# Performance work log

Hardware: AMD Instinct MI355X
Metric: run time of the kernel (lower is better)

Reference implementation:

```python
import jax, jax.numpy as jnp
import numpy as np

N_HEADS = 16
N_KV_HEADS = 4
WINDOW = 128
THETA = 10000.0


def _rope_cos_sin(T, half):
    inv = 1.0 / (THETA ** (jnp.arange(half, dtype=jnp.float32) / half))
    f = jnp.arange(T, dtype=jnp.float32)[:, None] * inv[None, :]  # (T, half)
    return jnp.cos(f), jnp.sin(f)


def _apply_rope(x, cos, sin):
    # x: (B, H, T, hd); interleaved (real, imag) pairs like torch view_as_complex
    xr, xi = x[..., 0::2], x[..., 1::2]
    out_r = xr * cos - xi * sin
    out_i = xr * sin + xi * cos
    return jnp.stack([out_r, out_i], axis=-1).reshape(x.shape)


def setup_inputs() -> dict:
    key = jax.random.key(0)
    ks = jax.random.split(key, 6)
    B, T, C = 1, 4096, 2048
    kvC = (C // N_HEADS) * N_KV_HEADS
    return {
        "x": jax.random.normal(ks[0], (B, T, C), dtype=jnp.float32),
        "wq": jax.random.normal(ks[1], (C, C), dtype=jnp.float32) * 0.02,
        "wk": jax.random.normal(ks[2], (C, kvC), dtype=jnp.float32) * 0.02,
        "wv": jax.random.normal(ks[3], (C, kvC), dtype=jnp.float32) * 0.02,
        "wo": jax.random.normal(ks[4], (C, C), dtype=jnp.float32) * 0.02,
        "sink": jnp.zeros((1, N_HEADS, 1, 1), dtype=jnp.float32),
    }


def reference(x, wq, wk, wv, wo, sink):
    B, T, C = x.shape
    hd = C // N_HEADS
    n_rep = N_HEADS // N_KV_HEADS

    q = (x @ wq).reshape(B, T, N_HEADS, hd).transpose(0, 2, 1, 3)    # (B,H,T,hd)
    k = (x @ wk).reshape(B, T, N_KV_HEADS, hd).transpose(0, 2, 1, 3)  # (B,Hkv,T,hd)
    v = (x @ wv).reshape(B, T, N_KV_HEADS, hd).transpose(0, 2, 1, 3)

    cos, sin = _rope_cos_sin(T, hd // 2)  # (T, hd/2), broadcasts over (B,H,T,hd/2)
    q = _apply_rope(q, cos, sin)
    k = _apply_rope(k, cos, sin)

    # GQA head expansion (repeat_interleave over head dim)
    k = jnp.repeat(k, n_rep, axis=1)
    v = jnp.repeat(v, n_rep, axis=1)

    att = jnp.einsum("bhqd,bhkd->bhqk", q, k) * (hd ** -0.5) + sink

    # symmetric sliding-window band: |i - j| <= window//2
    idx = jnp.arange(T)
    band = jnp.abs(idx[:, None] - idx[None, :]) <= (WINDOW // 2)
    att = jnp.where(band[None, None, :, :], att, -jnp.inf)

    att = jax.nn.softmax(att, axis=-1)
    # torch code replaces NaN rows (fully-masked) with uniform; band always has diag so no-op
    att = jnp.where(jnp.isnan(att), 1.0 / T, att)

    out = jnp.einsum("bhqk,bhkd->bqhd", att, v).reshape(B, T, C)
    return out @ wo
```

## Files before the change

### kernel.cpp

```cpp
#include <hip/hip_runtime.h>
#include <stdint.h>

#define T_SEQ 4096
#define C_DIM 2048
#define HD 128

typedef unsigned short ushort_t;
typedef __attribute__((ext_vector_type(8))) short shortx8;
typedef __attribute__((ext_vector_type(4))) float floatx4;
typedef __attribute__((ext_vector_type(8))) unsigned short u16x8;
typedef __attribute__((ext_vector_type(4))) unsigned short u16x4;

__device__ __forceinline__ ushort_t f2bf(float f) {
  union { float f; uint32_t u; } v; v.f = f;
  v.u += 0x7fffu + ((v.u >> 16) & 1u);
  return (ushort_t)(v.u >> 16);
}
__device__ __forceinline__ void load_lds16(const ushort_t* g, ushort_t* l) {
  __builtin_amdgcn_global_load_lds(
      (const __attribute__((address_space(1))) unsigned int*)g,
      (__attribute__((address_space(3))) unsigned int*)l, 16, 0, 0);
}

__global__ __launch_bounds__(256) void transpose_cvt(
    const float* __restrict__ src, ushort_t* __restrict__ dst, int R, int C) {
  __shared__ float tile[64][65];
  const int c0 = blockIdx.x * 64, r0 = blockIdx.y * 64;
  const int tid = threadIdx.x;
  for (int i = tid; i < 1024; i += 256) {
    int r = i >> 4, cc = (i & 15) * 4;
    float4 v = *(const float4*)&src[(size_t)(r0 + r) * C + c0 + cc];
    tile[r][cc] = v.x; tile[r][cc + 1] = v.y; tile[r][cc + 2] = v.z; tile[r][cc + 3] = v.w;
  }
  __syncthreads();
  for (int i = tid; i < 512; i += 256) {
    int oc = i >> 3;
    int g = (i & 7) * 8;
    u16x8 o;
    for (int j = 0; j < 8; ++j) o[j] = f2bf(tile[g + j][oc]);
    *(u16x8*)&dst[(size_t)(c0 + oc) * R + r0 + g] = o;
  }
}

__global__ __launch_bounds__(256) void cvt_bf16(
    const float* __restrict__ src, ushort_t* __restrict__ dst, int n4) {
  int i = blockIdx.x * 256 + threadIdx.x;
  if (i >= n4) return;
  float4 v = ((const float4*)src)[i];
  u16x4 o; o[0] = f2bf(v.x); o[1] = f2bf(v.y); o[2] = f2bf(v.z); o[3] = f2bf(v.w);
  ((u16x4*)dst)[i] = o;
}

__global__ __launch_bounds__(256, 3) void gemm_qkv(
    const ushort_t* __restrict__ A, const ushort_t* __restrict__ Bt,
    ushort_t* __restrict__ qbb, ushort_t* __restrict__ kbb,
    ushort_t* __restrict__ vtb) {
  __shared__ __align__(16) ushort_t As[128 * 32];
  __shared__ __align__(16) ushort_t Bs[128 * 32];
  const int tid = threadIdx.x;
  const int lane = tid & 63;
  const int wave = tid >> 6;
  const int quad = lane >> 4;
  const int l16 = lane & 15;
  const int m0 = blockIdx.y * 128;
  const int n0 = blockIdx.x * 128;
  const int wm = (wave & 1) * 64;
  const int wn = (wave >> 1) * 64;
  const int K = 2048;

  floatx4 acc[4][4] = {};

  int a_off[4], b_off[4];
  const int sfrag = (quad + ((l16 >> 1) & 3)) & 3;
  for (int i = 0; i < 4; ++i) {
    a_off[i] = (wm + i * 16 + l16) * 32 + sfrag * 8;
    b_off[i] = (wn + i * 16 + l16) * 32 + sfrag * 8;
  }

  for (int kk = 0; kk < 64; ++kk) {
    const int k0 = kk << 5;
    for (int r = 0; r < 2; ++r) {
      int c = r * 256 + tid;
      int row = c >> 2;
      int s = c & 3;
      int g = (s - (row >> 1)) & 3;
      const ushort_t* ga = A + (size_t)(m0 + row) * K + k0 + g * 8;
      const ushort_t* gb = Bt + (size_t)(n0 + row) * K + k0 + g * 8;
      ushort_t* la = As + (size_t)(r * 256 + (tid & 192)) * 8;
      ushort_t* lb = Bs + (size_t)(r * 256 + (tid & 192)) * 8;
      load_lds16(ga, la);
      load_lds16(gb, lb);
    }
    __syncthreads();
    shortx8 af[4], bfr[4];
    for (int i = 0; i < 4; ++i) {
      af[i] = *(const shortx8*)(As + a_off[i]);
      bfr[i] = *(const shortx8*)(Bs + b_off[i]);
    }
    for (int i = 0; i < 4; ++i)
      for (int j = 0; j < 4; ++j)
        acc[i][j] = __builtin_amdgcn_mfma_f32_16x16x32_bf16(af[i], bfr[j], acc[i][j], 0, 0, 0);
    __syncthreads();
  }

  if (blockIdx.x < 20) {
    const bool isq = (blockIdx.x < 16);
    const int par = l16 & 1;
    for (int j = 0; j < 4; ++j) {
      int col = n0 + wn + j * 16 + l16;
      int irot = (col & 127) >> 1;
      float inv = __expf(-0.14391157f * (float)irot);
      for (int i = 0; i < 4; ++i) {
        int t0r = m0 + wm + i * 16 + quad * 4;
        for (int r = 0; r < 4; ++r) {
          float val = acc[i][j][r];
          float other = __shfl_xor(val, 1, 64);
          float sn, cs;
          __sincosf((float)(t0r + r) * inv, &sn, &cs);
          float outv = par ? (other * sn + val * cs) : (val * cs - other * sn);
          if (isq) qbb[(size_t)(t0r + r) * 2048 + col] = f2bf(outv);
          else     kbb[(size_t)(t0r + r) * 512 + (col - 2048)] = f2bf(outv);
        }
      }
    }
  } else {
    for (int j = 0; j < 4; ++j) {
      int dim = n0 + wn + j * 16 + l16 - 2560;
      for (int i = 0; i < 4; ++i) {
        int t0r = m0 + wm + i * 16 + quad * 4;
        u16x4 o;
        for (int r = 0; r < 4; ++r) o[r] = f2bf(acc[i][j][r]);
        *(u16x4*)&vtb[(size_t)dim * T_SEQ + t0r] = o;
      }
    }
  }
}

__global__ __launch_bounds__(256, 3) void gemm_bf16(
    const ushort_t* __restrict__ A, const ushort_t* __restrict__ Bt,
    float* __restrict__ C, int M, int N, int K) {
  __shared__ __align__(16) ushort_t As[128 * 32];
  __shared__ __align__(16) ushort_t Bs[128 * 32];
  const int tid = threadIdx.x;
  const int lane = tid & 63;
  const int wave = tid >> 6;
  const int quad = lane >> 4;
  const int l16 = lane & 15;
  const int m0 = blockIdx.y * 128;
  const int n0 = blockIdx.x * 128;
  const int wm = (wave & 1) * 64;
  const int wn = (wave >> 1) * 64;

  floatx4 acc[4][4] = {};

  int a_off[4], b_off[4];
  const int sfrag = (quad + ((l16 >> 1) & 3)) & 3;
  for (int i = 0; i < 4; ++i) {
    a_off[i] = (wm + i * 16 + l16) * 32 + sfrag * 8;
    b_off[i] = (wn + i * 16 + l16) * 32 + sfrag * 8;
  }

  const int nk = K >> 5;
  for (int kk = 0; kk < nk; ++kk) {
    const int k0 = kk << 5;
    for (int r = 0; r < 2; ++r) {
      int c = r * 256 + tid;
      int row = c >> 2;
      int s = c & 3;
      int g = (s - (row >> 1)) & 3;
      const ushort_t* ga = A + (size_t)(m0 + row) * K + k0 + g * 8;
      const ushort_t* gb = Bt + (size_t)(n0 + row) * K + k0 + g * 8;
      ushort_t* la = As + (size_t)(r * 256 + (tid & 192)) * 8;
      ushort_t* lb = Bs + (size_t)(r * 256 + (tid & 192)) * 8;
      load_lds16(ga, la);
      load_lds16(gb, lb);
    }
    __syncthreads();
    shortx8 af[4], bfr[4];
    for (int i = 0; i < 4; ++i) {
      af[i] = *(const shortx8*)(As + a_off[i]);
      bfr[i] = *(const shortx8*)(Bs + b_off[i]);
    }
    for (int i = 0; i < 4; ++i)
      for (int j = 0; j < 4; ++j)
        acc[i][j] = __builtin_amdgcn_mfma_f32_16x16x32_bf16(af[i], bfr[j], acc[i][j], 0, 0, 0);
    __syncthreads();
  }
  for (int i = 0; i < 4; ++i)
    for (int j = 0; j < 4; ++j) {
      int col = n0 + wn + j * 16 + l16;
      int rbase = m0 + wm + i * 16 + quad * 4;
      for (int r = 0; r < 4; ++r)
        C[(size_t)(rbase + r) * N + col] = acc[i][j][r];
    }
}

__global__ __launch_bounds__(256, 3) void attn_kernel(
    const ushort_t* __restrict__ qbb, const ushort_t* __restrict__ kbb,
    const ushort_t* __restrict__ vtb, ushort_t* __restrict__ ao) {
  __shared__ __align__(16) ushort_t QP[32 * 160];
  __shared__ __align__(16) ushort_t KV[160 * 136];
  __shared__ float redmax[2][32];
  __shared__ float redsum[2][32];

  const int tid = threadIdx.x;
  const int lane = tid & 63;
  const int wave = tid >> 6;
  const int l16 = lane & 15;
  const int quad = lane >> 4;
  const int h = blockIdx.x;
  const int kvh = h >> 2;
  const int t0 = blockIdx.y * 32;
  const int kstart = t0 - 64;
  const int qh = wave & 1;
  const int khalf = wave >> 1;
  const float scale = 0.08838834764831845f;

  for (int c = tid; c < 512; c += 256) {
    int row = c >> 4, c8 = c & 15;
    u16x8 v = *(const u16x8*)&qbb[(size_t)(t0 + row) * C_DIM + h * HD + c8 * 8];
    *(u16x8*)&QP[row * 136 + c8 * 8] = v;
  }
  for (int c = tid; c < 2560; c += 256) {
    int row = c >> 4, c8 = c & 15;
    int t = kstart + row;
    u16x8 v;
    if (t >= 0 && t < T_SEQ) {
      v = *(const u16x8*)&kbb[(size_t)t * 512 + kvh * HD + c8 * 8];
    } else {
      for (int z = 0; z < 8; ++z) v[z] = 0;
    }
    *(u16x8*)&KV[row * 136 + c8 * 8] = v;
  }
  __syncthreads();

  floatx4 acc[5] = {};
  const int arow = qh * 16 + l16;
  for (int ks = 0; ks < 4; ++ks) {
    shortx8 af = *(const shortx8*)&QP[arow * 136 + ks * 32 + quad * 8];
    for (int kt = 0; kt < 5; ++kt) {
      int brow = khalf * 80 + kt * 16 + l16;
      shortx8 bf = *(const shortx8*)&KV[brow * 136 + ks * 32 + quad * 8];
      acc[kt] = __builtin_amdgcn_mfma_f32_16x16x32_bf16(af, bf, acc[kt], 0, 0, 0);
    }
  }

  float mrow[4] = {-3e38f, -3e38f, -3e38f, -3e38f};
  for (int kt = 0; kt < 5; ++kt) {
    int col = khalf * 80 + kt * 16 + l16;
    int kg = kstart + col;
    for (int r = 0; r < 4; ++r) {
      int row = qh * 16 + quad * 4 + r;
      bool valid = (kg >= 0) && (kg < T_SEQ) && (col >= row) && (col <= row + 128);
      float s = valid ? acc[kt][r] * scale : -3e38f;
      acc[kt][r] = s;
      mrow[r] = fmaxf(mrow[r], s);
    }
  }
  for (int off = 1; off < 16; off <<= 1)
    for (int r = 0; r < 4; ++r)
      mrow[r] = fmaxf(mrow[r], __shfl_xor(mrow[r], off, 64));
  if (l16 == 0)
    for (int r = 0; r < 4; ++r)
      redmax[khalf][qh * 16 + quad * 4 + r] = mrow[r];
  __syncthreads();

  float sum4[4];
  for (int r = 0; r < 4; ++r) {
    int row = qh * 16 + quad * 4 + r;
    float m = fmaxf(redmax[0][row], redmax[1][row]);
    float s = 0.f;
    for (int kt = 0; kt < 5; ++kt) {
      float p = expf(acc[kt][r] - m);
      acc[kt][r] = p;
      s += p;
    }
    sum4[r] = s;
  }
  for (int off = 1; off < 16; off <<= 1)
    for (int r = 0; r < 4; ++r) sum4[r] += __shfl_xor(sum4[r], off, 64);
  if (l16 == 0)
    for (int r = 0; r < 4; ++r)
      redsum[khalf][qh * 16 + quad * 4 + r] = sum4[r];

  for (int kt = 0; kt < 5; ++kt) {
    int col = khalf * 80 + kt * 16 + l16;
    for (int r = 0; r < 4; ++r) {
      int row = qh * 16 + quad * 4 + r;
      QP[row * 160 + col] = f2bf(acc[kt][r]);
    }
  }

  for (int c = tid; c < 2560; c += 256) {
    int row = c / 20, c8 = c % 20;
    int k0 = kstart + c8 * 8;
    const ushort_t* g = &vtb[(size_t)(kvh * HD + row) * T_SEQ];
    u16x8 v;
    if (k0 >= 0 && k0 + 7 < T_SEQ) {
      v = *(const u16x8*)&g[k0];
    } else {
      for (int z = 0; z < 8; ++z) {
        int kk = k0 + z;
        v[z] = (kk >= 0 && kk < T_SEQ) ? g[kk] : (ushort_t)0;
      }
    }
    *(u16x8*)&KV[row * 160 + c8 * 8] = v;
  }
  __syncthreads();

  floatx4 oacc[4] = {};
  const int prow = qh * 16 + l16;
  for (int ks = 0; ks < 5; ++ks) {
    shortx8 pf = *(const shortx8*)&QP[prow * 160 + ks * 32 + quad * 8];
    for (int dt = 0; dt < 4; ++dt) {
      int vrow = khalf * 64 + dt * 16 + l16;
      shortx8 vf = *(const shortx8*)&KV[vrow * 160 + ks * 32 + quad * 8];
      oacc[dt] = __builtin_amdgcn_mfma_f32_16x16x32_bf16(pf, vf, oacc[dt], 0, 0, 0);
    }
  }

  for (int r = 0; r < 4; ++r) {
    int row = qh * 16 + quad * 4 + r;
    float rl = 1.0f / (redsum[0][row] + redsum[1][row]);
    for (int dt = 0; dt < 4; ++dt) {
      int dim = khalf * 64 + dt * 16 + l16;
      ao[(size_t)(t0 + row) * C_DIM + h * HD + dim] = f2bf(oacc[dt][r] * rl);
    }
  }
}

extern "C" void kernel_launch(void* const* d_in, const int* in_sizes, int n_in,
                              void* d_out, int out_size, void* d_ws, size_t ws_size,
                              hipStream_t stream) {
  const float* x  = (const float*)d_in[0];
  const float* wq = (const float*)d_in[1];
  const float* wk = (const float*)d_in[2];
  const float* wv = (const float*)d_in[3];
  const float* wo = (const float*)d_in[4];
  float* out = (float*)d_out;

  char* ws = (char*)d_ws;
  ushort_t* BtAll = (ushort_t*)(ws);
  ushort_t* woT   = (ushort_t*)(ws + 12582912);
  ushort_t* xb    = (ushort_t*)(ws + 20971520);
  ushort_t* qbb   = (ushort_t*)(ws + 37748736);
  ushort_t* kbb   = (ushort_t*)(ws + 54525952);
  ushort_t* vtb   = (ushort_t*)(ws + 58720256);
  ushort_t* ao    = (ushort_t*)(ws + 62914560);

  transpose_cvt<<<dim3(32, 32), 256, 0, stream>>>(wq, BtAll, 2048, 2048);
  transpose_cvt<<<dim3(8, 32), 256, 0, stream>>>(wk, BtAll + (size_t)2048 * 2048, 2048, 512);
  transpose_cvt<<<dim3(8, 32), 256, 0, stream>>>(wv, BtAll + (size_t)2560 * 2048, 2048, 512);
  transpose_cvt<<<dim3(32, 32), 256, 0, stream>>>(wo, woT, 2048, 2048);
  cvt_bf16<<<8192, 256, 0, stream>>>(x, xb, 2097152);

  gemm_qkv<<<dim3(24, 32), 256, 0, stream>>>(xb, BtAll, qbb, kbb, vtb);

  attn_kernel<<<dim3(16, 128), 256, 0, stream>>>(qbb, kbb, vtb, ao);

  gemm_bf16<<<dim3(16, 32), 256, 0, stream>>>(ao, woT, out, 4096, 2048, 2048);
}
```

Measured before the change: 286.5 us.

## Merge prep launches into one kernel and double GEMM K-tile to 64

Five weight/input conversion launches are combined into a single prep kernel that dispatches on block index, removing per-launch gaps. Both GEMMs now share a core that stages a 64-wide K slice per iteration, with a new 8-way XOR-style LDS swizzle, so the loop runs half as many iterations and barrier pairs. The cost is double the LDS per block (32 KB), which may limit occupancy under the 3-blocks-per-CU launch bound. The prep kernel still allocates the transpose tile for x-conversion blocks that never use it.

```diff
diff --git a/kernel.cpp b/kernel.cpp
--- a/kernel.cpp
+++ b/kernel.cpp
@@ -22,11 +22,30 @@
       (__attribute__((address_space(3))) unsigned int*)l, 16, 0, 0);
 }
 
-__global__ __launch_bounds__(256) void transpose_cvt(
-    const float* __restrict__ src, ushort_t* __restrict__ dst, int R, int C) {
+__global__ __launch_bounds__(256) void prep_kernel(
+    const float* __restrict__ wq, const float* __restrict__ wk,
+    const float* __restrict__ wv, const float* __restrict__ wo,
+    const float* __restrict__ x,
+    ushort_t* __restrict__ BtAll, ushort_t* __restrict__ woT,
+    ushort_t* __restrict__ xb) {
+  const int bid = blockIdx.x;
+  const int tid = threadIdx.x;
+  if (bid >= 2560) {
+    int i = (bid - 2560) * 256 + tid;
+    float4 v = ((const float4*)x)[i];
+    u16x4 o; o[0] = f2bf(v.x); o[1] = f2bf(v.y); o[2] = f2bf(v.z); o[3] = f2bf(v.w);
+    ((u16x4*)xb)[i] = o;
+    return;
+  }
+  const float* src; ushort_t* dst; int C, bx, by;
+  if (bid < 1024) { src = wq; dst = BtAll; C = 2048; bx = bid & 31; by = bid >> 5; }
+  else if (bid < 1280) { int b = bid - 1024; src = wk; dst = BtAll + (size_t)2048 * 2048; C = 512; bx = b & 7; by = b >> 3; }
+  else if (bid < 1536) { int b = bid - 1280; src = wv; dst = BtAll + (size_t)2560 * 2048; C = 512; bx = b & 7; by = b >> 3; }
+  else { int b = bid - 1536; src = wo; dst = woT; C = 2048; bx = b & 31; by = b >> 5; }
+  const int R = 2048;
+
   __shared__ float tile[64][65];
-  const int c0 = blockIdx.x * 64, r0 = blockIdx.y * 64;
-  const int tid = threadIdx.x;
+  const int c0 = bx * 64, r0 = by * 64;
   for (int i = tid; i < 1024; i += 256) {
     int r = i >> 4, cc = (i & 15) * 4;
     float4 v = *(const float4*)&src[(size_t)(r0 + r) * C + c0 + cc];
@@ -42,21 +61,52 @@
   }
 }
 
-__global__ __launch_bounds__(256) void cvt_bf16(
-    const float* __restrict__ src, ushort_t* __restrict__ dst, int n4) {
-  int i = blockIdx.x * 256 + threadIdx.x;
-  if (i >= n4) return;
-  float4 v = ((const float4*)src)[i];
-  u16x4 o; o[0] = f2bf(v.x); o[1] = f2bf(v.y); o[2] = f2bf(v.z); o[3] = f2bf(v.w);
-  ((u16x4*)dst)[i] = o;
+
+struct GemmAcc { floatx4 a[4][4]; };
+
+__device__ __forceinline__ void gemm_core_bk64(
+    const ushort_t* __restrict__ A, const ushort_t* __restrict__ Bt,
+    ushort_t* As, ushort_t* Bs, GemmAcc& acc,
+    int m0, int n0, int K, int tid, int lane, int wave, int quad, int l16,
+    int wm, int wn) {
+  const int nk = K >> 6;
+  for (int kk = 0; kk < nk; ++kk) {
+    const int k0 = kk << 6;
+    for (int r = 0; r < 4; ++r) {
+      int e = r * 256 + tid;
+      int row = e >> 3;
+      int p = e & 7;
+      int g = (p - row) & 7;
+      const ushort_t* ga = A + (size_t)(m0 + row) * K + k0 + g * 8;
+      const ushort_t* gb = Bt + (size_t)(n0 + row) * K + k0 + g * 8;
+      ushort_t* la = As + (size_t)(r * 256 + (tid & 192)) * 8;
+      ushort_t* lb = Bs + (size_t)(r * 256 + (tid & 192)) * 8;
+      load_lds16(ga, la);
+      load_lds16(gb, lb);
+    }
+    __syncthreads();
+    for (int ks = 0; ks < 2; ++ks) {
+      shortx8 af[4], bfr[4];
+      for (int i = 0; i < 4; ++i) {
+        int ar = wm + i * 16 + l16;
+        af[i] = *(const shortx8*)(As + ar * 64 + (((ks << 2) + quad + ar) & 7) * 8);
+        int br = wn + i * 16 + l16;
+        bfr[i] = *(const shortx8*)(Bs + br * 64 + (((ks << 2) + quad + br) & 7) * 8);
+      }
+      for (int i = 0; i < 4; ++i)
+        for (int j = 0; j < 4; ++j)
+          acc.a[i][j] = __builtin_amdgcn_mfma_f32_16x16x32_bf16(af[i], bfr[j], acc.a[i][j], 0, 0, 0);
+    }
+    __syncthreads();
+  }
 }
 
 __global__ __launch_bounds__(256, 3) void gemm_qkv(
     const ushort_t* __restrict__ A, const ushort_t* __restrict__ Bt,
     ushort_t* __restrict__ qbb, ushort_t* __restrict__ kbb,
     ushort_t* __restrict__ vtb) {
-  __shared__ __align__(16) ushort_t As[128 * 32];
-  __shared__ __align__(16) ushort_t Bs[128 * 32];
+  __shared__ __align__(16) ushort_t As[128 * 64];
+  __shared__ __align__(16) ushort_t Bs[128 * 64];
   const int tid = threadIdx.x;
   const int lane = tid & 63;
   const int wave = tid >> 6;
@@ -66,42 +116,9 @@
   const int n0 = blockIdx.x * 128;
   const int wm = (wave & 1) * 64;
   const int wn = (wave >> 1) * 64;
-  const int K = 2048;
-
-  floatx4 acc[4][4] = {};
-
-  int a_off[4], b_off[4];
-  const int sfrag = (quad + ((l16 >> 1) & 3)) & 3;
-  for (int i = 0; i < 4; ++i) {
-    a_off[i] = (wm + i * 16 + l16) * 32 + sfrag * 8;
-    b_off[i] = (wn + i * 16 + l16) * 32 + sfrag * 8;
-  }
-
-  for (int kk = 0; kk < 64; ++kk) {
-    const int k0 = kk << 5;
-    for (int r = 0; r < 2; ++r) {
-      int c = r * 256 + tid;
-      int row = c >> 2;
-      int s = c & 3;
-      int g = (s - (row >> 1)) & 3;
-      const ushort_t* ga = A + (size_t)(m0 + row) * K + k0 + g * 8;
-      const ushort_t* gb = Bt + (size_t)(n0 + row) * K + k0 + g * 8;
-      ushort_t* la = As + (size_t)(r * 256 + (tid & 192)) * 8;
-      ushort_t* lb = Bs + (size_t)(r * 256 + (tid & 192)) * 8;
-      load_lds16(ga, la);
-      load_lds16(gb, lb);
-    }
-    __syncthreads();
-    shortx8 af[4], bfr[4];
-    for (int i = 0; i < 4; ++i) {
-      af[i] = *(const shortx8*)(As + a_off[i]);
-      bfr[i] = *(const shortx8*)(Bs + b_off[i]);
-    }
-    for (int i = 0; i < 4; ++i)
-      for (int j = 0; j < 4; ++j)
-        acc[i][j] = __builtin_amdgcn_mfma_f32_16x16x32_bf16(af[i], bfr[j], acc[i][j], 0, 0, 0);
-    __syncthreads();
-  }
+
+  GemmAcc acc = {};
+  gemm_core_bk64(A, Bt, As, Bs, acc, m0, n0, 2048, tid, lane, wave, quad, l16, wm, wn);
 
   if (blockIdx.x < 20) {
     const bool isq = (blockIdx.x < 16);
@@ -113,7 +130,7 @@
       for (int i = 0; i < 4; ++i) {
         int t0r = m0 + wm + i * 16 + quad * 4;
         for (int r = 0; r < 4; ++r) {
-          float val = acc[i][j][r];
+          float val = acc.a[i][j][r];
           float other = __shfl_xor(val, 1, 64);
           float sn, cs;
           __sincosf((float)(t0r + r) * inv, &sn, &cs);
@@ -129,7 +146,7 @@
       for (int i = 0; i < 4; ++i) {
         int t0r = m0 + wm + i * 16 + quad * 4;
         u16x4 o;
-        for (int r = 0; r < 4; ++r) o[r] = f2bf(acc[i][j][r]);
+        for (int r = 0; r < 4; ++r) o[r] = f2bf(acc.a[i][j][r]);
         *(u16x4*)&vtb[(size_t)dim * T_SEQ + t0r] = o;
       }
     }
@@ -139,8 +156,8 @@
 __global__ __launch_bounds__(256, 3) void gemm_bf16(
     const ushort_t* __restrict__ A, const ushort_t* __restrict__ Bt,
     float* __restrict__ C, int M, int N, int K) {
-  __shared__ __align__(16) ushort_t As[128 * 32];
-  __shared__ __align__(16) ushort_t Bs[128 * 32];
+  __shared__ __align__(16) ushort_t As[128 * 64];
+  __shared__ __align__(16) ushort_t Bs[128 * 64];
   const int tid = threadIdx.x;
   const int lane = tid & 63;
   const int wave = tid >> 6;
@@ -151,47 +168,15 @@
   const int wm = (wave & 1) * 64;
   const int wn = (wave >> 1) * 64;
 
-  floatx4 acc[4][4] = {};
-
-  int a_off[4], b_off[4];
-  const int sfrag = (quad + ((l16 >> 1) & 3)) & 3;
-  for (int i = 0; i < 4; ++i) {
-    a_off[i] = (wm + i * 16 + l16) * 32 + sfrag * 8;
-    b_off[i] = (wn + i * 16 + l16) * 32 + sfrag * 8;
-  }
-
-  const int nk = K >> 5;
-  for (int kk = 0; kk < nk; ++kk) {
-    const int k0 = kk << 5;
-    for (int r = 0; r < 2; ++r) {
-      int c = r * 256 + tid;
-      int row = c >> 2;
-      int s = c & 3;
-      int g = (s - (row >> 1)) & 3;
-      const ushort_t* ga = A + (size_t)(m0 + row) * K + k0 + g * 8;
-      const ushort_t* gb = Bt + (size_t)(n0 + row) * K + k0 + g * 8;
-      ushort_t* la = As + (size_t)(r * 256 + (tid & 192)) * 8;
-      ushort_t* lb = Bs + (size_t)(r * 256 + (tid & 192)) * 8;
-      load_lds16(ga, la);
-      load_lds16(gb, lb);
-    }
-    __syncthreads();
-    shortx8 af[4], bfr[4];
-    for (int i = 0; i < 4; ++i) {
-      af[i] = *(const shortx8*)(As + a_off[i]);
-      bfr[i] = *(const shortx8*)(Bs + b_off[i]);
-    }
-    for (int i = 0; i < 4; ++i)
-      for (int j = 0; j < 4; ++j)
-        acc[i][j] = __builtin_amdgcn_mfma_f32_16x16x32_bf16(af[i], bfr[j], acc[i][j], 0, 0, 0);
-    __syncthreads();
-  }
+  GemmAcc acc = {};
+  gemm_core_bk64(A, Bt, As, Bs, acc, m0, n0, K, tid, lane, wave, quad, l16, wm, wn);
+
   for (int i = 0; i < 4; ++i)
     for (int j = 0; j < 4; ++j) {
       int col = n0 + wn + j * 16 + l16;
       int rbase = m0 + wm + i * 16 + quad * 4;
       for (int r = 0; r < 4; ++r)
-        C[(size_t)(rbase + r) * N + col] = acc[i][j][r];
+        C[(size_t)(rbase + r) * N + col] = acc.a[i][j][r];
     }
 }
 
@@ -348,11 +333,7 @@
   ushort_t* vtb   = (ushort_t*)(ws + 58720256);
   ushort_t* ao    = (ushort_t*)(ws + 62914560);
 
-  transpose_cvt<<<dim3(32, 32), 256, 0, stream>>>(wq, BtAll, 2048, 2048);
-  transpose_cvt<<<dim3(8, 32), 256, 0, stream>>>(wk, BtAll + (size_t)2048 * 2048, 2048, 512);
-  transpose_cvt<<<dim3(8, 32), 256, 0, stream>>>(wv, BtAll + (size_t)2560 * 2048, 2048, 512);
-  transpose_cvt<<<dim3(32, 32), 256, 0, stream>>>(wo, woT, 2048, 2048);
-  cvt_bf16<<<8192, 256, 0, stream>>>(x, xb, 2097152);
+  prep_kernel<<<10752, 256, 0, stream>>>(wq, wk, wv, wo, x, BtAll, woT, xb);
 
   gemm_qkv<<<dim3(24, 32), 256, 0, stream>>>(xb, BtAll, qbb, kbb, vtb);
 
```

Result: faster. 263.3 us (-8.1%).
